# Performance work log

Hardware: AMD Instinct MI355X
Metric: run time of the kernel (lower is better)

The kernel has to match this reference:

```python
import jax, jax.numpy as jnp
import numpy as np
import math

NTOKEN = 32000; D = 512; H = 8; DFF = 2048; L = 4; B = 4; S = 1024; EPS = 1e-5


def _ln(x, g, b):
    m = x.mean(-1, keepdims=True)
    v = ((x - m) ** 2).mean(-1, keepdims=True)
    return (x - m) * jax.lax.rsqrt(v + EPS) * g + b


def setup_inputs() -> dict:
    key = jax.random.key(0)
    ks = jax.random.split(key, 20)
    s = 0.02
    rn = lambda k, shape: jax.random.normal(k, shape, jnp.float32) * s
    return {
        "src": jax.random.randint(ks[0], (B, S), 0, NTOKEN, jnp.int32),
        "emb": rn(ks[1], (NTOKEN, D)),
        "conv_w": rn(ks[2], (D, 1, 3)), "conv_b": rn(ks[3], (D,)),
        "bn_g": jnp.ones((D,)), "bn_b": jnp.zeros((D,)),
        "bn_m": jnp.zeros((D,)), "bn_v": jnp.ones((D,)),
        "w_ih": rn(ks[4], (4 * D, D)), "w_hh": rn(ks[5], (4 * D, D)),
        "b_ih": rn(ks[6], (4 * D,)), "b_hh": rn(ks[7], (4 * D,)),
        "in_w": rn(ks[8], (L, 3 * D, D)), "in_b": rn(ks[9], (L, 3 * D)),
        "out_w": rn(ks[10], (L, D, D)), "out_b": rn(ks[11], (L, D)),
        "ln1_g": jnp.ones((L, D)), "ln1_b": jnp.zeros((L, D)),
        "w1": rn(ks[12], (L, DFF, D)), "b1": rn(ks[13], (L, DFF)),
        "w2": rn(ks[14], (L, D, DFF)), "b2": rn(ks[15], (L, D)),
        "ln2_g": jnp.ones((L, D)), "ln2_b": jnp.zeros((L, D)),
        "fin_g": jnp.ones((D,)), "fin_b": jnp.zeros((D,)),
    }


def _forward(src, emb, conv_w, conv_b, bn_g, bn_b, bn_m, bn_v,
             w_ih, w_hh, b_ih, b_hh, in_w, in_b, out_w, out_b,
             ln1_g, ln1_b, w1, b1, w2, b2, ln2_g, ln2_b, fin_g, fin_b):
    d = emb.shape[1]
    x = emb[src] * math.sqrt(d)  # [B,S,D]
    # sinusoidal positional encoding (dropout is identity at eval)
    pos = jnp.arange(S, dtype=jnp.float32)[:, None]
    div = jnp.exp(jnp.arange(0, d, 2, dtype=jnp.float32) * (-math.log(10000.0) / d))
    pe = jnp.zeros((S, d), jnp.float32)
    pe = pe.at[:, 0::2].set(jnp.sin(pos * div)).at[:, 1::2].set(jnp.cos(pos * div))
    x = x + pe[None]
    # depthwise conv k=3 + BatchNorm1d (eval stats) + ReLU
    xc = jnp.transpose(x, (0, 2, 1))  # [B,D,S]
    xc = jax.lax.conv_general_dilated(xc, conv_w, (1,), [(1, 1)],
                                      feature_group_count=d,
                                      dimension_numbers=('NCH', 'OIH', 'NCH'))
    xc = xc + conv_b[None, :, None]
    xc = (xc - bn_m[None, :, None]) * jax.lax.rsqrt(bn_v + EPS)[None, :, None] \
         * bn_g[None, :, None] + bn_b[None, :, None]
    x = jnp.transpose(jax.nn.relu(xc), (0, 2, 1))
    # single-layer LSTM (torch gate order i,f,g,o)
    def step(carry, xt):
        h, c = carry
        gates = xt @ w_ih.T + b_ih + h @ w_hh.T + b_hh
        i, f, g, o = jnp.split(gates, 4, axis=-1)
        c = jax.nn.sigmoid(f) * c + jax.nn.sigmoid(i) * jnp.tanh(g)
        h = jax.nn.sigmoid(o) * jnp.tanh(c)
        return (h, c), h
    h0 = jnp.zeros((x.shape[0], d), x.dtype)
    _, hs = jax.lax.scan(step, (h0, h0), jnp.transpose(x, (1, 0, 2)))
    x = x + jnp.transpose(hs, (1, 0, 2))
    # post-norm encoder layers, attn weights averaged over heads
    hd = d // H
    scale = 1.0 / math.sqrt(hd)
    attns = []
    out = x
    for l in range(L):
        qkv = out @ in_w[l].T + in_b[l]
        q, k, v = jnp.split(qkv, 3, axis=-1)
        q = q.reshape(B, S, H, hd).transpose(0, 2, 1, 3) * scale
        k = k.reshape(B, S, H, hd).transpose(0, 2, 1, 3)
        v = v.reshape(B, S, H, hd).transpose(0, 2, 1, 3)
        a = jax.nn.softmax(jnp.einsum('bhqd,bhkd->bhqk', q, k), axis=-1)
        attns.append(a.mean(axis=1))  # averaged over heads, as need_weights=True default
        ctx = jnp.einsum('bhqk,bhkd->bhqd', a, v).transpose(0, 2, 1, 3).reshape(B, S, d)
        out = _ln(out + ctx @ out_w[l].T + out_b[l], ln1_g[l], ln1_b[l])
        ff = jax.nn.gelu(out @ w1[l].T + b1[l], approximate=False) @ w2[l].T + b2[l]
        out = _ln(out + ff, ln2_g[l], ln2_b[l])
    return _ln(out, fin_g, fin_b), jnp.stack(attns)


def reference(src, emb, conv_w, conv_b, bn_g, bn_b, bn_m, bn_v,
              w_ih, w_hh, b_ih, b_hh, in_w, in_b, out_w, out_b,
              ln1_g, ln1_b, w1, b1, w2, b2, ln2_g, ln2_b, fin_g, fin_b):
    return _forward(src, emb, conv_w, conv_b, bn_g, bn_b, bn_m, bn_v,
                    w_ih, w_hh, b_ih, b_hh, in_w, in_b, out_w, out_b,
                    ln1_g, ln1_b, w1, b1, w2, b2, ln2_g, ln2_b, fin_g, fin_b)
```

## Files before the change

kernel.cpp:

```cpp
#include <hip/hip_runtime.h>
#include <math.h>

#define DD 512
#define SS 1024
#define BB 4
#define HH 8
#define DFF 2048
#define LL 4
#define NT 4096
#define EPSF 1e-5f

#define O_X0    ((size_t)0)
#define O_X1    ((size_t)2097152)
#define O_HSEQ  ((size_t)4194304)
#define O_CTX   ((size_t)6293504)
#define O_QKV   ((size_t)8390656)
#define O_BIG   ((size_t)14682112)
#define O_BSUM  ((size_t)31459328)

typedef unsigned int  u32;
typedef unsigned short u16;
typedef __attribute__((ext_vector_type(8))) _Float16 f16x8;
typedef __attribute__((ext_vector_type(4))) _Float16 f16x4;
typedef __attribute__((ext_vector_type(4))) float    f32x4;

__device__ __forceinline__ float fsig(float x){
  return __builtin_amdgcn_rcpf(1.0f + __expf(-x));
}
__device__ __forceinline__ float ftanh(float x){
  return 1.0f - 2.0f*__builtin_amdgcn_rcpf(1.0f + __expf(2.0f*x));
}
union f16u { u16 u; _Float16 f; };
__device__ __forceinline__ float b2f(u16 b){ f16u t; t.u = b; return (float)t.f; }
__device__ __forceinline__ u16 f2b(_Float16 h){ f16u t; t.f = h; return t.u; }
__device__ __forceinline__ u32 pack2(float v){
  _Float16 hi = (_Float16)v;
  _Float16 lo = (_Float16)(v - (float)hi);
  return (u32)f2b(hi) | ((u32)f2b(lo) << 16);
}

__global__ void k_embed(const int* __restrict__ src, const float* __restrict__ emb,
                        float* __restrict__ x){
  int idx = blockIdx.x*256 + threadIdx.x;
  if (idx >= NT*DD) return;
  int d = idx & (DD-1);
  int n = idx >> 9;
  int s = n & (SS-1);
  int tok = src[n];
  int i2 = d & ~1;
  float div = expf(-(float)i2 * (9.210340371976184f/512.0f));
  float ang = (float)s * div;
  float pe = (d & 1) ? cosf(ang) : sinf(ang);
  x[idx] = emb[(size_t)tok*DD + d]*22.62741699796952f + pe;
}

__global__ void k_conv(const float* __restrict__ x, const float* __restrict__ cw,
                       const float* __restrict__ cb, const float* __restrict__ bg,
                       const float* __restrict__ bb, const float* __restrict__ bm,
                       const float* __restrict__ bv, float* __restrict__ y,
                       u32* __restrict__ yp){
  int idx = blockIdx.x*256 + threadIdx.x;
  if (idx >= NT*DD) return;
  int d = idx & (DD-1);
  int n = idx >> 9;
  int s = n & (SS-1);
  float acc = cb[d];
  if (s > 0)     acc += x[idx - DD]*cw[d*3+0];
  acc += x[idx]*cw[d*3+1];
  if (s < SS-1)  acc += x[idx + DD]*cw[d*3+2];
  float v = (acc - bm[d])*rsqrtf(bv[d]+EPSF)*bg[d] + bb[d];
  v = fmaxf(v, 0.0f);
  y[idx] = v;
  yp[idx] = pack2(v);
}

__global__ void k_bsum(const float* a, const float* b, float* o, int n){
  int i = blockIdx.x*256 + threadIdx.x;
  if (i < n) o[i] = a[i] + b[i];
}

__global__ void k_wsplit(const float* __restrict__ W, u32* __restrict__ Wp, int total){
  int i = blockIdx.x*1024 + threadIdx.x*4;
  if (i >= total) return;
  float4 v = *reinterpret_cast<const float4*>(W + i);
  uint4 o;
  o.x = pack2(v.x); o.y = pack2(v.y); o.z = pack2(v.z); o.w = pack2(v.w);
  *reinterpret_cast<uint4*>(Wp + i) = o;
}

__global__ void k_wsplit_qkv(const float* __restrict__ inw, const float* __restrict__ inb,
                             u32* __restrict__ Wq, float* __restrict__ qbias){
  size_t i = (size_t)blockIdx.x*1024 + threadIdx.x*4;
  float s = (i < 262144) ? 0.125f : 1.0f;
  float4 v = *reinterpret_cast<const float4*>(inw + i);
  uint4 o;
  o.x = pack2(v.x*s); o.y = pack2(v.y*s); o.z = pack2(v.z*s); o.w = pack2(v.w*s);
  *reinterpret_cast<uint4*>(Wq + i) = o;
  if (blockIdx.x == 0){
    for (int j = threadIdx.x; j < 1536; j += 256){
      float bv = inb[j];
      qbias[j] = (j < 512) ? bv*0.125f : bv;
    }
  }
}

__global__ void k_wsplit_post(const float* __restrict__ outw, const float* __restrict__ w1,
                              const float* __restrict__ w2,
                              u32* __restrict__ Wo, u32* __restrict__ W1p,
                              u32* __restrict__ W2p){
  size_t i = (size_t)blockIdx.x*1024 + threadIdx.x*4;
  const float* src; u32* dst; size_t off;
  if (i < 262144){ src = outw; dst = Wo; off = i; }
  else if (i < 1310720){ src = w1; dst = W1p; off = i - 262144; }
  else { src = w2; dst = W2p; off = i - 1310720; }
  float4 v = *reinterpret_cast<const float4*>(src + off);
  uint4 o;
  o.x = pack2(v.x); o.y = pack2(v.y); o.z = pack2(v.z); o.w = pack2(v.w);
  *reinterpret_cast<uint4*>(dst + off) = o;
}

__device__ __forceinline__ void unpk4(uint4 w, uint2& hi, uint2& lo){
  hi.x = (w.x & 0xffffu) | (w.y << 16);
  hi.y = (w.z & 0xffffu) | (w.w << 16);
  lo.x = (w.x >> 16) | (w.y & 0xffff0000u);
  lo.y = (w.z >> 16) | (w.w & 0xffff0000u);
}
__device__ __forceinline__ uint2 unpk4hi(uint4 w){
  uint2 hi;
  hi.x = (w.x & 0xffffu) | (w.y << 16);
  hi.y = (w.z & 0xffffu) | (w.w << 16);
  return hi;
}

#define BKP 40
template<int ACT, int OSPLIT>
__global__ __launch_bounds__(256) void k_gemm_mfma(const u32* __restrict__ Ain,
                                                   const u32* __restrict__ Wp,
                                                   const float* __restrict__ bias,
                                                   void* __restrict__ Cout,
                                                   int M, int N, int K){
  __shared__ _Float16 Ah[128][BKP];
  __shared__ _Float16 Wh[128][BKP];
  __shared__ _Float16 Wl[128][BKP];
  const int tid = threadIdx.x;
  const int nbx = N >> 7;
  const int bx = blockIdx.x % nbx;
  const int by = blockIdx.x / nbx;
  const int m0 = by << 7, n0 = bx << 7;
  const int lane = tid & 63;
  const int wid  = tid >> 6;
  const int wr = wid >> 1, wc = wid & 1;
  const int fm = lane & 15, fg = lane >> 4;
  const int r0 = tid >> 3;
  const int k4 = (tid & 7) << 2;
  const u32* Wbase = Wp + (size_t)(n0 + r0)*K + k4;
  const u32* Abase = Ain + (size_t)(m0 + r0)*K + k4;

  f32x4 acc[4][4];
  #pragma unroll
  for (int i=0;i<4;i++)
    #pragma unroll
    for (int j=0;j<4;j++) acc[i][j] = (f32x4){0.0f,0.0f,0.0f,0.0f};

  uint4 rw[4], ra4[4];
  #pragma unroll
  for (int e=0;e<4;e++){
    rw[e]  = *reinterpret_cast<const uint4*>(Wbase + (size_t)(e*32)*K);
    ra4[e] = *reinterpret_cast<const uint4*>(Abase + (size_t)(e*32)*K);
  }

  for (int k0 = 0; k0 < K; k0 += 32){
    #pragma unroll
    for (int e = 0; e < 4; ++e){
      int rr = r0 + e*32;
      uint2 hi, lo;
      unpk4(rw[e], hi, lo);
      *reinterpret_cast<uint2*>(&Wh[rr][k4]) = hi;
      *reinterpret_cast<uint2*>(&Wl[rr][k4]) = lo;
      *reinterpret_cast<uint2*>(&Ah[rr][k4]) = unpk4hi(ra4[e]);
    }
    __syncthreads();
    if (k0 + 32 < K){
      #pragma unroll
      for (int e=0;e<4;e++){
        rw[e]  = *reinterpret_cast<const uint4*>(Wbase + (size_t)(e*32)*K + k0 + 32);
        ra4[e] = *reinterpret_cast<const uint4*>(Abase + (size_t)(e*32)*K + k0 + 32);
      }
    }
    f16x8 a_h[4], w_h[4], w_l[4];
    #pragma unroll
    for (int i=0;i<4;i++){
      int row = wr*64 + i*16 + fm;
      a_h[i] = *reinterpret_cast<const f16x8*>(&Ah[row][fg*8]);
    }
    #pragma unroll
    for (int j=0;j<4;j++){
      int row = wc*64 + j*16 + fm;
      w_h[j] = *reinterpret_cast<const f16x8*>(&Wh[row][fg*8]);
      w_l[j] = *reinterpret_cast<const f16x8*>(&Wl[row][fg*8]);
    }
    #pragma unroll
    for (int i=0;i<4;i++)
      #pragma unroll
      for (int j=0;j<4;j++){
        acc[i][j] = __builtin_amdgcn_mfma_f32_16x16x32_f16(a_h[i], w_h[j], acc[i][j], 0, 0, 0);
        acc[i][j] = __builtin_amdgcn_mfma_f32_16x16x32_f16(a_h[i], w_l[j], acc[i][j], 0, 0, 0);
      }
    __syncthreads();
  }
  #pragma unroll
  for (int i=0;i<4;i++){
    #pragma unroll
    for (int r=0;r<4;r++){
      int row = m0 + wr*64 + i*16 + fg*4 + r;
      #pragma unroll
      for (int j=0;j<4;j++){
        int col = n0 + wc*64 + j*16 + fm;
        float v = acc[i][j][r] + bias[col];
        if (ACT == 1) v = 0.5f*v*(1.0f + erff(v*0.70710678118654752f));
        if constexpr (OSPLIT) ((u32*)Cout)[(size_t)row*N + col] = pack2(v);
        else                  ((float*)Cout)[(size_t)row*N + col] = v;
      }
    }
  }
}

template<int ACT, int OSPLIT>
__global__ __launch_bounds__(256) void k_gemm64_mfma(const u32* __restrict__ Ain,
                                                     const u32* __restrict__ Wp,
                                                     const float* __restrict__ bias,
                                                     void* __restrict__ Cout,
                                                     int M, int N, int K){
  __shared__ _Float16 Ah[128][BKP];
  __shared__ _Float16 Wh[64][BKP];
  __shared__ _Float16 Wl[64][BKP];
  const int tid = threadIdx.x;
  const int nbx = N >> 6;
  const int bx = blockIdx.x % nbx;
  const int by = blockIdx.x / nbx;
  const int m0 = by << 7, n0 = bx << 6;
  const int lane = tid & 63;
  const int wid  = tid >> 6;
  const int wr = wid >> 1, wc = wid & 1;
  const int fm = lane & 15, fg = lane >> 4;
  const int r0 = tid >> 3;
  const int k4 = (tid & 7) << 2;
  const u32* Wbase = Wp + (size_t)(n0 + r0)*K + k4;
  const u32* Abase = Ain + (size_t)(m0 + r0)*K + k4;

  f32x4 acc[4][2];
  #pragma unroll
  for (int i=0;i<4;i++){ acc[i][0] = (f32x4){0,0,0,0}; acc[i][1] = (f32x4){0,0,0,0}; }

  uint4 rw[2], ra4[4];
  #pragma unroll
  for (int e=0;e<2;e++)
    rw[e]  = *reinterpret_cast<const uint4*>(Wbase + (size_t)(e*32)*K);
  #pragma unroll
  for (int e=0;e<4;e++)
    ra4[e] = *reinterpret_cast<const uint4*>(Abase + (size_t)(e*32)*K);

  for (int k0 = 0; k0 < K; k0 += 32){
    #pragma unroll
    for (int e = 0; e < 2; ++e){
      int rr = r0 + e*32;
      uint2 hi, lo;
      unpk4(rw[e], hi, lo);
      *reinterpret_cast<uint2*>(&Wh[rr][k4]) = hi;
      *reinterpret_cast<uint2*>(&Wl[rr][k4]) = lo;
    }
    #pragma unroll
    for (int e = 0; e < 4; ++e){
      int rr = r0 + e*32;
      *reinterpret_cast<uint2*>(&Ah[rr][k4]) = unpk4hi(ra4[e]);
    }
    __syncthreads();
    if (k0 + 32 < K){
      #pragma unroll
      for (int e=0;e<2;e++)
        rw[e]  = *reinterpret_cast<const uint4*>(Wbase + (size_t)(e*32)*K + k0 + 32);
      #pragma unroll
      for (int e=0;e<4;e++)
        ra4[e] = *reinterpret_cast<const uint4*>(Abase + (size_t)(e*32)*K + k0 + 32);
    }
    f16x8 a_h[4], w_h[2], w_l[2];
    #pragma unroll
    for (int i=0;i<4;i++){
      int row = wr*64 + i*16 + fm;
      a_h[i] = *reinterpret_cast<const f16x8*>(&Ah[row][fg*8]);
    }
    #pragma unroll
    for (int j=0;j<2;j++){
      int row = wc*32 + j*16 + fm;
      w_h[j] = *reinterpret_cast<const f16x8*>(&Wh[row][fg*8]);
      w_l[j] = *reinterpret_cast<const f16x8*>(&Wl[row][fg*8]);
    }
    #pragma unroll
    for (int i=0;i<4;i++)
      #pragma unroll
      for (int j=0;j<2;j++){
        acc[i][j] = __builtin_amdgcn_mfma_f32_16x16x32_f16(a_h[i], w_h[j], acc[i][j], 0, 0, 0);
        acc[i][j] = __builtin_amdgcn_mfma_f32_16x16x32_f16(a_h[i], w_l[j], acc[i][j], 0, 0, 0);
      }
    __syncthreads();
  }
  #pragma unroll
  for (int i=0;i<4;i++){
    #pragma unroll
    for (int r=0;r<4;r++){
      int row = m0 + wr*64 + i*16 + fg*4 + r;
      #pragma unroll
      for (int j=0;j<2;j++){
        int col = n0 + wc*32 + j*16 + fm;
        float v = acc[i][j][r] + bias[col];
        if (ACT == 1) v = 0.5f*v*(1.0f + erff(v*0.70710678118654752f));
        if constexpr (OSPLIT) ((u32*)Cout)[(size_t)row*N + col] = pack2(v);
        else                  ((float*)Cout)[(size_t)row*N + col] = v;
      }
    }
  }
}

#define SPAD 72
__global__ __launch_bounds__(256) void k_scores_mfma(const u32* __restrict__ qkv,
                                                     u16* __restrict__ sc){
  __shared__ _Float16 Qh[128][SPAD];
  __shared__ _Float16 Kh[128][SPAD], Kl[128][SPAD];
  const int tid = threadIdx.x;
  const int kt = blockIdx.x & 7;
  const int qt = (blockIdx.x >> 3) & 7;
  const int h  = (blockIdx.x >> 6) & 7;
  const int b  = (blockIdx.x >> 9) & 3;
  const int q0 = qt*128, k0 = kt*128;
  #pragma unroll
  for (int e=0;e<8;e++){
    int lin = e*256 + tid;
    int rr = lin >> 4;
    int c4 = (lin & 15) << 2;
    uint4 qv = *reinterpret_cast<const uint4*>(qkv + (size_t)(b*SS + q0+rr)*1536 + h*64 + c4);
    uint4 kv = *reinterpret_cast<const uint4*>(qkv + (size_t)(b*SS + k0+rr)*1536 + DD + h*64 + c4);
    uint2 hi, lo;
    *reinterpret_cast<uint2*>(&Qh[rr][c4]) = unpk4hi(qv);
    unpk4(kv, hi, lo);
    *reinterpret_cast<uint2*>(&Kh[rr][c4]) = hi;
    *reinterpret_cast<uint2*>(&Kl[rr][c4]) = lo;
  }
  __syncthreads();
  const int lane = tid & 63, wid = tid >> 6;
  const int wr = wid >> 1, wc = wid & 1;
  const int fm = lane & 15, fg = lane >> 4;
  f32x4 acc[4][4];
  #pragma unroll
  for (int i=0;i<4;i++)
    #pragma unroll
    for (int j=0;j<4;j++) acc[i][j] = (f32x4){0.0f,0.0f,0.0f,0.0f};
  #pragma unroll
  for (int ks=0; ks<2; ks++){
    f16x8 ah[4], bh[4], bl[4];
    #pragma unroll
    for (int i=0;i<4;i++){
      int row = wr*64 + i*16 + fm;
      ah[i] = *reinterpret_cast<const f16x8*>(&Qh[row][ks*32 + fg*8]);
    }
    #pragma unroll
    for (int j=0;j<4;j++){
      int row = wc*64 + j*16 + fm;
      bh[j] = *reinterpret_cast<const f16x8*>(&Kh[row][ks*32 + fg*8]);
      bl[j] = *reinterpret_cast<const f16x8*>(&Kl[row][ks*32 + fg*8]);
    }
    #pragma unroll
    for (int i=0;i<4;i++)
      #pragma unroll
      for (int j=0;j<4;j++){
        acc[i][j] = __builtin_amdgcn_mfma_f32_16x16x32_f16(ah[i], bh[j], acc[i][j], 0, 0, 0);
        acc[i][j] = __builtin_amdgcn_mfma_f32_16x16x32_f16(ah[i], bl[j], acc[i][j], 0, 0, 0);
      }
  }
  u16* out = sc + (size_t)(b*HH + h)*SS*SS;
  #pragma unroll
  for (int i=0;i<4;i++){
    #pragma unroll
    for (int r=0;r<4;r++){
      int row = q0 + wr*64 + i*16 + fg*4 + r;
      #pragma unroll
      for (int j=0;j<4;j++){
        int col = k0 + wc*64 + j*16 + fm;
        out[(size_t)row*SS + col] = f2b((_Float16)acc[i][j][r]);
      }
    }
  }
}

__global__ __launch_bounds__(256) void k_pv_mfma(const u16* __restrict__ sc,
                                                 const u32* __restrict__ qkv,
                                                 u32* __restrict__ ctx){
  __shared__ _Float16 Ph[64][SPAD];
  __shared__ _Float16 Vh[64][SPAD],  Vl[64][SPAD];
  const int tid = threadIdx.x;
  const int qt = blockIdx.x & 15;
  const int h  = (blockIdx.x >> 4) & 7;
  const int b  = (blockIdx.x >> 7) & 3;
  const int q0 = qt*64;
  const u16* Pb = sc + (size_t)(b*HH + h)*SS*SS;
  const int lane = tid & 63, wid = tid >> 6;
  const int wr = wid >> 1, wc = wid & 1;
  const int fm = lane & 15, fg = lane >> 4;
  const int pr0 = tid >> 4;
  const int pc4 = (tid & 15) << 2;
  const int vd  = tid & 63;
  const int vk0 = tid >> 6;
  const u16* Pbase = Pb + (size_t)(q0 + pr0)*SS + pc4;
  const u32* Vbase = qkv + (size_t)(b*SS + vk0)*1536 + 1024 + h*64 + vd;
  f32x4 acc[2][2];
  #pragma unroll
  for (int i=0;i<2;i++){ acc[i][0] = (f32x4){0,0,0,0}; acc[i][1] = (f32x4){0,0,0,0}; }

  uint2 rp[4];
  u32   rv[16];
  #pragma unroll
  for (int e=0;e<4;e++)  rp[e] = *reinterpret_cast<const uint2*>(Pbase + (size_t)(e*16)*SS);
  #pragma unroll
  for (int e=0;e<16;e++) rv[e] = Vbase[(size_t)(e*4)*1536];

  for (int kk0=0; kk0<SS; kk0+=64){
    #pragma unroll
    for (int e=0;e<4;e++){
      int rr = pr0 + e*16;
      *reinterpret_cast<uint2*>(&Ph[rr][pc4]) = rp[e];
    }
    #pragma unroll
    for (int e=0;e<16;e++){
      int k = vk0 + e*4;
      u32 w = rv[e];
      f16u thi, tlo; thi.u = (u16)w; tlo.u = (u16)(w >> 16);
      Vh[vd][k] = thi.f;
      Vl[vd][k] = tlo.f;
    }
    __syncthreads();
    if (kk0 + 64 < SS){
      #pragma unroll
      for (int e=0;e<4;e++)
        rp[e] = *reinterpret_cast<const uint2*>(Pbase + (size_t)(e*16)*SS + kk0 + 64);
      #pragma unroll
      for (int e=0;e<16;e++)
        rv[e] = Vbase[(size_t)(kk0 + 64 + e*4)*1536];
    }
    #pragma unroll
    for (int ks=0; ks<2; ks++){
      f16x8 ah[2], bh[2], bl[2];
      #pragma unroll
      for (int i=0;i<2;i++){
        int row = wr*32 + i*16 + fm;
        ah[i] = *reinterpret_cast<const f16x8*>(&Ph[row][ks*32 + fg*8]);
      }
      #pragma unroll
      for (int j=0;j<2;j++){
        int row = wc*32 + j*16 + fm;
        bh[j] = *reinterpret_cast<const f16x8*>(&Vh[row][ks*32 + fg*8]);
        bl[j] = *reinterpret_cast<const f16x8*>(&Vl[row][ks*32 + fg*8]);
      }
      #pragma unroll
      for (int i=0;i<2;i++)
        #pragma unroll
        for (int j=0;j<2;j++){
          acc[i][j] = __builtin_amdgcn_mfma_f32_16x16x32_f16(ah[i], bh[j], acc[i][j], 0, 0, 0);
          acc[i][j] = __builtin_amdgcn_mfma_f32_16x16x32_f16(ah[i], bl[j], acc[i][j], 0, 0, 0);
        }
    }
    __syncthreads();
  }
  #pragma unroll
  for (int i=0;i<2;i++){
    #pragma unroll
    for (int r=0;r<4;r++){
      int row = q0 + wr*32 + i*16 + fg*4 + r;
      #pragma unroll
      for (int j=0;j<2;j++){
        int col = wc*32 + j*16 + fm;
        ctx[(size_t)(b*SS + row)*DD + h*64 + col] = pack2(acc[i][j][r]);
      }
    }
  }
}

__global__ __launch_bounds__(256) void k_lstm(const float* __restrict__ gates_in,
                                              const float* __restrict__ w_hh,
                                              unsigned long long* __restrict__ hpack){
  __shared__ float hsh[2][8][68];
  const int b = blockIdx.x >> 6;
  const int chunk = blockIdx.x & 63;
  const int d0 = chunk*8;
  const int tid = threadIdx.x;
  const int wave = tid >> 6;
  const int lane = tid & 63;
  const int diw = lane >> 5;
  const int g   = (lane >> 3) & 3;
  const int ks  = lane & 7;
  const int dim = wave*2 + diw;
  const int src0 = diw*32;
  float w[64];
  {
    const float* wrow = w_hh + (size_t)(g*DD + d0 + dim)*DD;
// ... 41 lines not shown
    float acc = (a0+a1)+(a2+a3);
    acc += __shfl_down(acc, 4, 8);
    acc += __shfl_down(acc, 2, 8);
    acc += __shfl_down(acc, 1, 8);
    float v = acc + gv;
    float gval = (g == 2) ? ftanh(v) : fsig(v);
    float gi = __shfl(gval, src0 + 0);
    float gf = __shfl(gval, src0 + 8);
    float gg = __shfl(gval, src0 + 16);
    float go = __shfl(gval, src0 + 24);
    c = gf*c + gi*gg;
    float h = go*ftanh(c);
    if (lane == src0){
      union { float f; unsigned int u; } hu; hu.f = h;
      unsigned long long pk = ((unsigned long long)(unsigned int)(t+1) << 32)
                            | (unsigned long long)hu.u;
      __hip_atomic_store(&hpack[(size_t)((t+1)*BB + b)*DD + d0 + dim], pk,
                         __ATOMIC_RELAXED, __HIP_MEMORY_SCOPE_AGENT);
    }
  }
}

__global__ void k_resid(float* __restrict__ x, const unsigned long long* __restrict__ hpack,
                        u32* __restrict__ xp){
  int idx = blockIdx.x*256 + threadIdx.x;
  if (idx >= NT*DD) return;
  int d = idx & (DD-1);
  int n = idx >> 9;
  int s = n & (SS-1);
  int b = n >> 10;
  union { unsigned int u; float f; } hu;
  hu.u = (unsigned int)hpack[(size_t)((s+1)*BB + b)*DD + d];
  float v = x[idx] + hu.f;
  x[idx] = v;
  xp[idx] = pack2(v);
}

__global__ __launch_bounds__(256) void k_softmax(u16* __restrict__ sc,
                                                 float* __restrict__ attn_out,
                                                 int l){
  __shared__ float avgw[4][SS];
  const int tid = threadIdx.x;
  const int q  = blockIdx.x & (SS-1);
  const int b  = blockIdx.x >> 10;
  const int wave = tid >> 6, lane = tid & 63;
  #pragma unroll
  for (int j=0;j<16;j++) avgw[wave][j*64 + lane] = 0.0f;
  #pragma unroll
  for (int hi=0; hi<2; hi++){
    int h = wave + hi*4;
    u16* row = sc + (size_t)(b*HH + h)*SS*SS + (size_t)q*SS;
    float v[16];
    float m = -1e30f;
    #pragma unroll
    for (int j=0;j<16;j++){ v[j] = b2f(row[j*64 + lane]); m = fmaxf(m, v[j]); }
    #pragma unroll
    for (int o=32;o>0;o>>=1) m = fmaxf(m, __shfl_xor(m, o));
    float s = 0.0f;
    #pragma unroll
    for (int j=0;j<16;j++){ v[j] = __expf(v[j] - m); s += v[j]; }
    #pragma unroll
    for (int o=32;o>0;o>>=1) s += __shfl_xor(s, o);
    float inv = __builtin_amdgcn_rcpf(s);
    #pragma unroll
    for (int j=0;j<16;j++){
      float p = v[j]*inv;
      row[j*64 + lane] = f2b((_Float16)p);
      avgw[wave][j*64 + lane] += p;
    }
  }
  __syncthreads();
  float* ao = attn_out + (size_t)((l*BB + b)*SS + q)*SS;
  for (int j=tid;j<SS;j+=256)
    ao[j] = (avgw[0][j]+avgw[1][j]+avgw[2][j]+avgw[3][j])*0.125f;
}

__global__ __launch_bounds__(64) void k_ln(const float* __restrict__ x,
                                           const float* __restrict__ y,
                                           const float* __restrict__ g,
                                           const float* __restrict__ bta,
                                           float* __restrict__ out,
                                           u32* __restrict__ outp){
  const int n = blockIdx.x;
  const int tid = threadIdx.x;
  float v[8];
  float s = 0.0f, sq = 0.0f;
  #pragma unroll
  for (int j=0;j<8;j++){
    int d = j*64 + tid;
    float a = x[(size_t)n*DD + d];
    if (y) a += y[(size_t)n*DD + d];
    v[j] = a; s += a; sq += a*a;
  }
  #pragma unroll
  for (int o=32;o>0;o>>=1){ s += __shfl_xor(s, o); sq += __shfl_xor(sq, o); }
  float mean = s*(1.0f/DD);
  float var = sq*(1.0f/DD) - mean*mean;
  float rstd = rsqrtf(var + EPSF);
  #pragma unroll
  for (int j=0;j<8;j++){
    int d = j*64 + tid;
    float r = (v[j]-mean)*rstd*g[d] + bta[d];
    out[(size_t)n*DD + d] = r;
    if (outp) outp[(size_t)n*DD + d] = pack2(r);
  }
}

extern "C" void kernel_launch(void* const* d_in, const int* in_sizes, int n_in,
                              void* d_out, int out_size, void* d_ws, size_t ws_size,
                              hipStream_t stream){
  const int*   src    = (const int*)  d_in[0];
  const float* emb    = (const float*)d_in[1];
  const float* conv_w = (const float*)d_in[2];
  const float* conv_b = (const float*)d_in[3];
  const float* bn_g   = (const float*)d_in[4];
  const float* bn_b   = (const float*)d_in[5];
  const float* bn_m   = (const float*)d_in[6];
  const float* bn_v   = (const float*)d_in[7];
  const float* w_ih   = (const float*)d_in[8];
  const float* w_hh   = (const float*)d_in[9];
  const float* b_ih   = (const float*)d_in[10];
  const float* b_hh   = (const float*)d_in[11];
  const float* in_w   = (const float*)d_in[12];
  const float* in_b   = (const float*)d_in[13];
  const float* out_w  = (const float*)d_in[14];
  const float* out_b  = (const float*)d_in[15];
  const float* ln1_g  = (const float*)d_in[16];
  const float* ln1_b  = (const float*)d_in[17];
  const float* w1     = (const float*)d_in[18];
  const float* b1     = (const float*)d_in[19];
  const float* w2     = (const float*)d_in[20];
  const float* b2     = (const float*)d_in[21];
  const float* ln2_g  = (const float*)d_in[22];
  const float* ln2_b  = (const float*)d_in[23];
  const float* fin_g  = (const float*)d_in[24];
  const float* fin_b  = (const float*)d_in[25];

  float* ws    = (float*)d_ws;
  float* x0    = ws + O_X0;
  float* x1    = ws + O_X1;
  float* ctx   = ws + O_CTX;
  float* qkv   = ws + O_QKV;
  float* big   = ws + O_BIG;
  float* bsum  = ws + O_BSUM;
  unsigned long long* hpack = (unsigned long long*)(big + 8388608);

  u32*   aconv = (u32*)(ws + O_HSEQ);
  float* qbias = ws + O_HSEQ + 2097152;
  u32*   qkvp  = (u32*)qkv;
  u32*   ctxp  = (u32*)ctx;
  u16*   sc16  = (u16*)big;
  u32*   wsg   = (u32*)(big + 13000000);
  u32*   Wq    = (u32*)(big + 8388608);
  u32*   Wo    = (u32*)(big + 8388608);
  u32*   W1p   = (u32*)(big + 8650752);
  u32*   W2p   = (u32*)(big + 9699328);

  float* outx  = (float*)d_out;
  float* attn  = outx + (size_t)NT*DD;

  hipMemsetAsync(hpack, 0, (size_t)(SS+1)*BB*DD*sizeof(unsigned long long), stream);

  const int eb = (NT*DD)/256;
  k_embed<<<eb, 256, 0, stream>>>(src, emb, x0);
  k_conv <<<eb, 256, 0, stream>>>(x0, conv_w, conv_b, bn_g, bn_b, bn_m, bn_v, x1, aconv);
  k_bsum <<<8, 256, 0, stream>>>(b_ih, b_hh, bsum, 4*DD);

  k_wsplit<<<1024, 256, 0, stream>>>(w_ih, wsg, 2048*512);
  k_gemm_mfma<0,0><<<(NT/128)*((4*DD)/128), 256, 0, stream>>>(
      aconv, wsg, bsum, big, NT, 4*DD, DD);
  k_lstm<<<256, 256, 0, stream>>>(big, w_hh, hpack);
  k_resid<<<eb, 256, 0, stream>>>(x1, hpack, aconv);

  float* cur = x1;
  float* tmp = x0;
  for (int l=0; l<LL; ++l){
    k_wsplit_qkv<<<768, 256, 0, stream>>>(in_w + (size_t)l*1536*DD,
                                          in_b + (size_t)l*1536, Wq, qbias);
    k_gemm_mfma<0,1><<<(NT/128)*(1536/128), 256, 0, stream>>>(
        aconv, Wq, qbias, qkvp, NT, 1536, DD);
    k_scores_mfma<<<2048, 256, 0, stream>>>(qkvp, sc16);
    k_softmax    <<<4096, 256, 0, stream>>>(sc16, attn, l);
    k_pv_mfma    <<<512,  256, 0, stream>>>(sc16, qkvp, ctxp);
    k_wsplit_post<<<2304, 256, 0, stream>>>(out_w + (size_t)l*DD*DD,
                                            w1 + (size_t)l*DFF*DD,
                                            w2 + (size_t)l*DD*DFF, Wo, W1p, W2p);
    k_gemm64_mfma<0,0><<<(NT/128)*(DD/64), 256, 0, stream>>>(
        ctxp, Wo, out_b + (size_t)l*DD, tmp, NT, DD, DD);
    k_ln<<<NT, 64, 0, stream>>>(cur, tmp, ln1_g + l*DD, ln1_b + l*DD, cur, aconv);
    k_gemm_mfma<1,1><<<(NT/128)*(DFF/128), 256, 0, stream>>>(
        aconv, W1p, b1 + (size_t)l*DFF, (u32*)big, NT, DFF, DD);
    k_gemm64_mfma<0,0><<<(NT/128)*(DD/64), 256, 0, stream>>>(
        (u32*)big, W2p, b2 + (size_t)l*DD, tmp, NT, DD, DFF);
    k_ln<<<NT, 64, 0, stream>>>(cur, tmp, ln2_g + l*DD, ln2_b + l*DD, cur, aconv);
  }
  k_ln<<<NT, 64, 0, stream>>>(cur, nullptr, fin_g, fin_b, outx, nullptr);
}
```

Measured before the change: 2.481 ms.

## Drop split-fp16 low parts for transformer GEMMs and attention, use plain fp16

Activations, QKV, context, FFN hidden and transformer weights are stored as single fp16 values instead of packed hi/lo fp16 pairs. The low-part MFMA passes in the attention and FFN GEMMs, scores and PV kernels are removed, which halves MFMA work and shared/global traffic for those stages. Only the LSTM input projection keeps a split-precision weight. The QKV GEMM also moves to the 64-wide tile kernel. Numerical accuracy falls to plain fp16 inputs with fp32 accumulation, which could exceed tolerance.

```diff
diff --git a/kernel.cpp b/kernel.cpp
--- a/kernel.cpp
+++ b/kernel.cpp
@@ -21,7 +21,6 @@
 typedef unsigned int  u32;
 typedef unsigned short u16;
 typedef __attribute__((ext_vector_type(8))) _Float16 f16x8;
-typedef __attribute__((ext_vector_type(4))) _Float16 f16x4;
 typedef __attribute__((ext_vector_type(4))) float    f32x4;
 
 __device__ __forceinline__ float fsig(float x){
@@ -37,6 +36,12 @@
   _Float16 hi = (_Float16)v;
   _Float16 lo = (_Float16)(v - (float)hi);
   return (u32)f2b(hi) | ((u32)f2b(lo) << 16);
+}
+__device__ __forceinline__ uint2 pk4h(float4 v, float s){
+  uint2 o;
+  o.x = (u32)f2b((_Float16)(v.x*s)) | ((u32)f2b((_Float16)(v.y*s)) << 16);
+  o.y = (u32)f2b((_Float16)(v.z*s)) | ((u32)f2b((_Float16)(v.w*s)) << 16);
+  return o;
 }
 
 __global__ void k_embed(const int* __restrict__ src, const float* __restrict__ emb,
@@ -58,7 +63,7 @@
                        const float* __restrict__ cb, const float* __restrict__ bg,
                        const float* __restrict__ bb, const float* __restrict__ bm,
                        const float* __restrict__ bv, float* __restrict__ y,
-                       u32* __restrict__ yp){
+                       u16* __restrict__ yp){
   int idx = blockIdx.x*256 + threadIdx.x;
   if (idx >= NT*DD) return;
   int d = idx & (DD-1);
@@ -71,7 +76,7 @@
   float v = (acc - bm[d])*rsqrtf(bv[d]+EPSF)*bg[d] + bb[d];
   v = fmaxf(v, 0.0f);
   y[idx] = v;
-  yp[idx] = pack2(v);
+  yp[idx] = f2b((_Float16)v);
 }
 
 __global__ void k_bsum(const float* a, const float* b, float* o, int n){
@@ -89,13 +94,11 @@
 }
 
 __global__ void k_wsplit_qkv(const float* __restrict__ inw, const float* __restrict__ inb,
-                             u32* __restrict__ Wq, float* __restrict__ qbias){
+                             u16* __restrict__ Wq, float* __restrict__ qbias){
   size_t i = (size_t)blockIdx.x*1024 + threadIdx.x*4;
   float s = (i < 262144) ? 0.125f : 1.0f;
   float4 v = *reinterpret_cast<const float4*>(inw + i);
-  uint4 o;
-  o.x = pack2(v.x*s); o.y = pack2(v.y*s); o.z = pack2(v.z*s); o.w = pack2(v.w*s);
-  *reinterpret_cast<uint4*>(Wq + i) = o;
+  *reinterpret_cast<uint2*>(Wq + i) = pk4h(v, s);
   if (blockIdx.x == 0){
     for (int j = threadIdx.x; j < 1536; j += 256){
       float bv = inb[j];
@@ -106,17 +109,15 @@
 
 __global__ void k_wsplit_post(const float* __restrict__ outw, const float* __restrict__ w1,
                               const float* __restrict__ w2,
-                              u32* __restrict__ Wo, u32* __restrict__ W1p,
-                              u32* __restrict__ W2p){
+                              u16* __restrict__ Wo, u16* __restrict__ W1p,
+                              u16* __restrict__ W2p){
   size_t i = (size_t)blockIdx.x*1024 + threadIdx.x*4;
-  const float* src; u32* dst; size_t off;
+  const float* src; u16* dst; size_t off;
   if (i < 262144){ src = outw; dst = Wo; off = i; }
   else if (i < 1310720){ src = w1; dst = W1p; off = i - 262144; }
   else { src = w2; dst = W2p; off = i - 1310720; }
   float4 v = *reinterpret_cast<const float4*>(src + off);
-  uint4 o;
-  o.x = pack2(v.x); o.y = pack2(v.y); o.z = pack2(v.z); o.w = pack2(v.w);
-  *reinterpret_cast<uint4*>(dst + off) = o;
+  *reinterpret_cast<uint2*>(dst + off) = pk4h(v, 1.0f);
 }
 
 __device__ __forceinline__ void unpk4(uint4 w, uint2& hi, uint2& lo){
@@ -125,20 +126,14 @@
   lo.x = (w.x >> 16) | (w.y & 0xffff0000u);
   lo.y = (w.z >> 16) | (w.w & 0xffff0000u);
 }
-__device__ __forceinline__ uint2 unpk4hi(uint4 w){
-  uint2 hi;
-  hi.x = (w.x & 0xffffu) | (w.y << 16);
-  hi.y = (w.z & 0xffffu) | (w.w << 16);
-  return hi;
-}
 
 #define BKP 40
-template<int ACT, int OSPLIT>
-__global__ __launch_bounds__(256) void k_gemm_mfma(const u32* __restrict__ Ain,
-                                                   const u32* __restrict__ Wp,
-                                                   const float* __restrict__ bias,
-                                                   void* __restrict__ Cout,
-                                                   int M, int N, int K){
+
+__global__ __launch_bounds__(256) void k_gemm2p(const u16* __restrict__ A,
+                                                const u32* __restrict__ Wp,
+                                                const float* __restrict__ bias,
+                                                float* __restrict__ C,
+                                                int M, int N, int K){
   __shared__ _Float16 Ah[128][BKP];
   __shared__ _Float16 Wh[128][BKP];
   __shared__ _Float16 Wl[128][BKP];
@@ -151,10 +146,12 @@
   const int wid  = tid >> 6;
   const int wr = wid >> 1, wc = wid & 1;
   const int fm = lane & 15, fg = lane >> 4;
-  const int r0 = tid >> 3;
-  const int k4 = (tid & 7) << 2;
-  const u32* Wbase = Wp + (size_t)(n0 + r0)*K + k4;
-  const u32* Abase = Ain + (size_t)(m0 + r0)*K + k4;
+  const int r0a = tid >> 2;
+  const int k8  = (tid & 3) << 3;
+  const int r0w = tid >> 3;
+  const int k4  = (tid & 7) << 2;
+  const u16* Abase = A + (size_t)(m0 + r0a)*K + k8;
+  const u32* Wbase = Wp + (size_t)(n0 + r0w)*K + k4;
 
   f32x4 acc[4][4];
   #pragma unroll
@@ -162,42 +159,40 @@
     #pragma unroll
     for (int j=0;j<4;j++) acc[i][j] = (f32x4){0.0f,0.0f,0.0f,0.0f};
 
-  uint4 rw[4], ra4[4];
-  #pragma unroll
-  for (int e=0;e<4;e++){
-    rw[e]  = *reinterpret_cast<const uint4*>(Wbase + (size_t)(e*32)*K);
-    ra4[e] = *reinterpret_cast<const uint4*>(Abase + (size_t)(e*32)*K);
-  }
+  uint4 ra[2], rw[4];
+  #pragma unroll
+  for (int e=0;e<2;e++) ra[e] = *reinterpret_cast<const uint4*>(Abase + (size_t)(e*64)*K);
+  #pragma unroll
+  for (int e=0;e<4;e++) rw[e] = *reinterpret_cast<const uint4*>(Wbase + (size_t)(e*32)*K);
 
   for (int k0 = 0; k0 < K; k0 += 32){
     #pragma unroll
-    for (int e = 0; e < 4; ++e){
-      int rr = r0 + e*32;
+    for (int e=0;e<2;e++)
+      *reinterpret_cast<uint4*>(&Ah[r0a + e*64][k8]) = ra[e];
+    #pragma unroll
+    for (int e=0;e<4;e++){
       uint2 hi, lo;
       unpk4(rw[e], hi, lo);
-      *reinterpret_cast<uint2*>(&Wh[rr][k4]) = hi;
-      *reinterpret_cast<uint2*>(&Wl[rr][k4]) = lo;
-      *reinterpret_cast<uint2*>(&Ah[rr][k4]) = unpk4hi(ra4[e]);
+      *reinterpret_cast<uint2*>(&Wh[r0w + e*32][k4]) = hi;
+      *reinterpret_cast<uint2*>(&Wl[r0w + e*32][k4]) = lo;
     }
     __syncthreads();
     if (k0 + 32 < K){
       #pragma unroll
-      for (int e=0;e<4;e++){
-        rw[e]  = *reinterpret_cast<const uint4*>(Wbase + (size_t)(e*32)*K + k0 + 32);
-        ra4[e] = *reinterpret_cast<const uint4*>(Abase + (size_t)(e*32)*K + k0 + 32);
-      }
+      for (int e=0;e<2;e++)
+        ra[e] = *reinterpret_cast<const uint4*>(Abase + (size_t)(e*64)*K + k0 + 32);
+      #pragma unroll
+      for (int e=0;e<4;e++)
+        rw[e] = *reinterpret_cast<const uint4*>(Wbase + (size_t)(e*32)*K + k0 + 32);
     }
     f16x8 a_h[4], w_h[4], w_l[4];
     #pragma unroll
-    for (int i=0;i<4;i++){
-      int row = wr*64 + i*16 + fm;
-      a_h[i] = *reinterpret_cast<const f16x8*>(&Ah[row][fg*8]);
-    }
+    for (int i=0;i<4;i++)
+      a_h[i] = *reinterpret_cast<const f16x8*>(&Ah[wr*64 + i*16 + fm][fg*8]);
     #pragma unroll
     for (int j=0;j<4;j++){
-      int row = wc*64 + j*16 + fm;
-      w_h[j] = *reinterpret_cast<const f16x8*>(&Wh[row][fg*8]);
-      w_l[j] = *reinterpret_cast<const f16x8*>(&Wl[row][fg*8]);
+      w_h[j] = *reinterpret_cast<const f16x8*>(&Wh[wc*64 + j*16 + fm][fg*8]);
+      w_l[j] = *reinterpret_cast<const f16x8*>(&Wl[wc*64 + j*16 + fm][fg*8]);
     }
     #pragma unroll
     for (int i=0;i<4;i++)
@@ -216,24 +211,100 @@
       #pragma unroll
       for (int j=0;j<4;j++){
         int col = n0 + wc*64 + j*16 + fm;
+        C[(size_t)row*N + col] = acc[i][j][r] + bias[col];
+      }
+    }
+  }
+}
+
+template<int ACT, int OHALF>
+__global__ __launch_bounds__(256) void k_gemmh(const u16* __restrict__ A,
+                                               const u16* __restrict__ W,
+                                               const float* __restrict__ bias,
+                                               void* __restrict__ Cout,
+                                               int M, int N, int K){
+  __shared__ _Float16 Ah[128][BKP];
+  __shared__ _Float16 Wh[128][BKP];
+  const int tid = threadIdx.x;
+  const int nbx = N >> 7;
+  const int bx = blockIdx.x % nbx;
+  const int by = blockIdx.x / nbx;
+  const int m0 = by << 7, n0 = bx << 7;
+  const int lane = tid & 63;
+  const int wid  = tid >> 6;
+  const int wr = wid >> 1, wc = wid & 1;
+  const int fm = lane & 15, fg = lane >> 4;
+  const int r0 = tid >> 2;
+  const int k8 = (tid & 3) << 3;
+  const u16* Abase = A + (size_t)(m0 + r0)*K + k8;
+  const u16* Wbase = W + (size_t)(n0 + r0)*K + k8;
+
+  f32x4 acc[4][4];
+  #pragma unroll
+  for (int i=0;i<4;i++)
+    #pragma unroll
+    for (int j=0;j<4;j++) acc[i][j] = (f32x4){0.0f,0.0f,0.0f,0.0f};
+
+  uint4 ra[2], rw[2];
+  #pragma unroll
+  for (int e=0;e<2;e++){
+    ra[e] = *reinterpret_cast<const uint4*>(Abase + (size_t)(e*64)*K);
+    rw[e] = *reinterpret_cast<const uint4*>(Wbase + (size_t)(e*64)*K);
+  }
+
+  for (int k0 = 0; k0 < K; k0 += 32){
+    #pragma unroll
+    for (int e=0;e<2;e++){
+      *reinterpret_cast<uint4*>(&Ah[r0 + e*64][k8]) = ra[e];
+      *reinterpret_cast<uint4*>(&Wh[r0 + e*64][k8]) = rw[e];
+    }
+    __syncthreads();
+    if (k0 + 32 < K){
+      #pragma unroll
+      for (int e=0;e<2;e++){
+        ra[e] = *reinterpret_cast<const uint4*>(Abase + (size_t)(e*64)*K + k0 + 32);
+        rw[e] = *reinterpret_cast<const uint4*>(Wbase + (size_t)(e*64)*K + k0 + 32);
+      }
+    }
+    f16x8 a_h[4], w_h[4];
+    #pragma unroll
+    for (int i=0;i<4;i++)
+      a_h[i] = *reinterpret_cast<const f16x8*>(&Ah[wr*64 + i*16 + fm][fg*8]);
+    #pragma unroll
+    for (int j=0;j<4;j++)
+      w_h[j] = *reinterpret_cast<const f16x8*>(&Wh[wc*64 + j*16 + fm][fg*8]);
+    #pragma unroll
+    for (int i=0;i<4;i++)
+      #pragma unroll
+      for (int j=0;j<4;j++)
+        acc[i][j] = __builtin_amdgcn_mfma_f32_16x16x32_f16(a_h[i], w_h[j], acc[i][j], 0, 0, 0);
+    __syncthreads();
+  }
+  #pragma unroll
+  for (int i=0;i<4;i++){
+    #pragma unroll
+    for (int r=0;r<4;r++){
+      int row = m0 + wr*64 + i*16 + fg*4 + r;
+      #pragma unroll
+      for (int j=0;j<4;j++){
+        int col = n0 + wc*64 + j*16 + fm;
         float v = acc[i][j][r] + bias[col];
         if (ACT == 1) v = 0.5f*v*(1.0f + erff(v*0.70710678118654752f));
-        if constexpr (OSPLIT) ((u32*)Cout)[(size_t)row*N + col] = pack2(v);
-        else                  ((float*)Cout)[(size_t)row*N + col] = v;
+        if constexpr (OHALF) ((u16*)Cout)[(size_t)row*N + col] = f2b((_Float16)v);
+        else                 ((float*)Cout)[(size_t)row*N + col] = v;
       }
     }
   }
 }
 
-template<int ACT, int OSPLIT>
-__global__ __launch_bounds__(256) void k_gemm64_mfma(const u32* __restrict__ Ain,
-                                                     const u32* __restrict__ Wp,
-                                                     const float* __restrict__ bias,
-                                                     void* __restrict__ Cout,
-                                                     int M, int N, int K){
+template<int ACT, int OHALF>
+__global__ __launch_bounds__(256) void k_gemm64h(const u16* __restrict__ A,
+                                                 const u16* __restrict__ W,
+                                                 const float* __restrict__ bias,
+                                                 void* __restrict__ Cout,
+                                                 int M, int N, int K){
   __shared__ _Float16 Ah[128][BKP];
   __shared__ _Float16 Wh[64][BKP];
-  __shared__ _Float16 Wl[64][BKP];
   const int tid = threadIdx.x;
   const int nbx = N >> 6;
   const int bx = blockIdx.x % nbx;
@@ -243,65 +314,45 @@
   const int wid  = tid >> 6;
   const int wr = wid >> 1, wc = wid & 1;
   const int fm = lane & 15, fg = lane >> 4;
-  const int r0 = tid >> 3;
-  const int k4 = (tid & 7) << 2;
-  const u32* Wbase = Wp + (size_t)(n0 + r0)*K + k4;
-  const u32* Abase = Ain + (size_t)(m0 + r0)*K + k4;
+  const int r0 = tid >> 2;
+  const int k8 = (tid & 3) << 3;
+  const u16* Abase = A + (size_t)(m0 + r0)*K + k8;
+  const u16* Wbase = W + (size_t)(n0 + r0)*K + k8;
 
   f32x4 acc[4][2];
   #pragma unroll
   for (int i=0;i<4;i++){ acc[i][0] = (f32x4){0,0,0,0}; acc[i][1] = (f32x4){0,0,0,0}; }
 
-  uint4 rw[2], ra4[4];
+  uint4 ra[2], rw0;
   #pragma unroll
   for (int e=0;e<2;e++)
-    rw[e]  = *reinterpret_cast<const uint4*>(Wbase + (size_t)(e*32)*K);
-  #pragma unroll
-  for (int e=0;e<4;e++)
-    ra4[e] = *reinterpret_cast<const uint4*>(Abase + (size_t)(e*32)*K);
+    ra[e] = *reinterpret_cast<const uint4*>(Abase + (size_t)(e*64)*K);
+  rw0 = *reinterpret_cast<const uint4*>(Wbase);
 
   for (int k0 = 0; k0 < K; k0 += 32){
     #pragma unroll
-    for (int e = 0; e < 2; ++e){
-      int rr = r0 + e*32;
-      uint2 hi, lo;
-      unpk4(rw[e], hi, lo);
-      *reinterpret_cast<uint2*>(&Wh[rr][k4]) = hi;
-      *reinterpret_cast<uint2*>(&Wl[rr][k4]) = lo;
-    }
-    #pragma unroll
-    for (int e = 0; e < 4; ++e){
-      int rr = r0 + e*32;
-      *reinterpret_cast<uint2*>(&Ah[rr][k4]) = unpk4hi(ra4[e]);
-    }
+    for (int e=0;e<2;e++)
+      *reinterpret_cast<uint4*>(&Ah[r0 + e*64][k8]) = ra[e];
+    *reinterpret_cast<uint4*>(&Wh[r0][k8]) = rw0;
     __syncthreads();
     if (k0 + 32 < K){
       #pragma unroll
       for (int e=0;e<2;e++)
-        rw[e]  = *reinterpret_cast<const uint4*>(Wbase + (size_t)(e*32)*K + k0 + 32);
-      #pragma unroll
-      for (int e=0;e<4;e++)
-        ra4[e] = *reinterpret_cast<const uint4*>(Abase + (size_t)(e*32)*K + k0 + 32);
-    }
-    f16x8 a_h[4], w_h[2], w_l[2];
-    #pragma unroll
-    for (int i=0;i<4;i++){
-      int row = wr*64 + i*16 + fm;
-      a_h[i] = *reinterpret_cast<const f16x8*>(&Ah[row][fg*8]);
-    }
-    #pragma unroll
-    for (int j=0;j<2;j++){
-      int row = wc*32 + j*16 + fm;
-      w_h[j] = *reinterpret_cast<const f16x8*>(&Wh[row][fg*8]);
-      w_l[j] = *reinterpret_cast<const f16x8*>(&Wl[row][fg*8]);
-    }
+        ra[e] = *reinterpret_cast<const uint4*>(Abase + (size_t)(e*64)*K + k0 + 32);
+      rw0 = *reinterpret_cast<const uint4*>(Wbase + k0 + 32);
+    }
+    f16x8 a_h[4], w_h[2];
     #pragma unroll
     for (int i=0;i<4;i++)
-      #pragma unroll
-      for (int j=0;j<2;j++){
+      a_h[i] = *reinterpret_cast<const f16x8*>(&Ah[wr*64 + i*16 + fm][fg*8]);
+    #pragma unroll
+    for (int j=0;j<2;j++)
+      w_h[j] = *reinterpret_cast<const f16x8*>(&Wh[wc*32 + j*16 + fm][fg*8]);
+    #pragma unroll
+    for (int i=0;i<4;i++)
+      #pragma unroll
+      for (int j=0;j<2;j++)
         acc[i][j] = __builtin_amdgcn_mfma_f32_16x16x32_f16(a_h[i], w_h[j], acc[i][j], 0, 0, 0);
-        acc[i][j] = __builtin_amdgcn_mfma_f32_16x16x32_f16(a_h[i], w_l[j], acc[i][j], 0, 0, 0);
-      }
     __syncthreads();
   }
   #pragma unroll
@@ -314,18 +365,18 @@
         int col = n0 + wc*32 + j*16 + fm;
         float v = acc[i][j][r] + bias[col];
         if (ACT == 1) v = 0.5f*v*(1.0f + erff(v*0.70710678118654752f));
-        if constexpr (OSPLIT) ((u32*)Cout)[(size_t)row*N + col] = pack2(v);
-        else                  ((float*)Cout)[(size_t)row*N + col] = v;
+        if constexpr (OHALF) ((u16*)Cout)[(size_t)row*N + col] = f2b((_Float16)v);
+        else                 ((float*)Cout)[(size_t)row*N + col] = v;
       }
     }
   }
 }
 
 #define SPAD 72
-__global__ __launch_bounds__(256) void k_scores_mfma(const u32* __restrict__ qkv,
+__global__ __launch_bounds__(256) void k_scores_mfma(const u16* __restrict__ qkv,
                                                      u16* __restrict__ sc){
   __shared__ _Float16 Qh[128][SPAD];
-  __shared__ _Float16 Kh[128][SPAD], Kl[128][SPAD];
+  __shared__ _Float16 Kh[128][SPAD];
   const int tid = threadIdx.x;
   const int kt = blockIdx.x & 7;
   const int qt = (blockIdx.x >> 3) & 7;
@@ -333,17 +384,14 @@
   const int b  = (blockIdx.x >> 9) & 3;
   const int q0 = qt*128, k0 = kt*128;
   #pragma unroll
-  for (int e=0;e<8;e++){
+  for (int e=0;e<4;e++){
     int lin = e*256 + tid;
-    int rr = lin >> 4;
-    int c4 = (lin & 15) << 2;
-    uint4 qv = *reinterpret_cast<const uint4*>(qkv + (size_t)(b*SS + q0+rr)*1536 + h*64 + c4);
-    uint4 kv = *reinterpret_cast<const uint4*>(qkv + (size_t)(b*SS + k0+rr)*1536 + DD + h*64 + c4);
-    uint2 hi, lo;
-    *reinterpret_cast<uint2*>(&Qh[rr][c4]) = unpk4hi(qv);
-    unpk4(kv, hi, lo);
-    *reinterpret_cast<uint2*>(&Kh[rr][c4]) = hi;
-    *reinterpret_cast<uint2*>(&Kl[rr][c4]) = lo;
+    int rr = lin >> 3;
+    int c8 = (lin & 7) << 3;
+    *reinterpret_cast<uint4*>(&Qh[rr][c8]) =
+      *reinterpret_cast<const uint4*>(qkv + (size_t)(b*SS + q0+rr)*1536 + h*64 + c8);
+    *reinterpret_cast<uint4*>(&Kh[rr][c8]) =
+      *reinterpret_cast<const uint4*>(qkv + (size_t)(b*SS + k0+rr)*1536 + DD + h*64 + c8);
   }
   __syncthreads();
   const int lane = tid & 63, wid = tid >> 6;
@@ -356,25 +404,18 @@
     for (int j=0;j<4;j++) acc[i][j] = (f32x4){0.0f,0.0f,0.0f,0.0f};
   #pragma unroll
   for (int ks=0; ks<2; ks++){
-    f16x8 ah[4], bh[4], bl[4];
-    #pragma unroll
-    for (int i=0;i<4;i++){
-      int row = wr*64 + i*16 + fm;
-      ah[i] = *reinterpret_cast<const f16x8*>(&Qh[row][ks*32 + fg*8]);
-    }
-    #pragma unroll
-    for (int j=0;j<4;j++){
-      int row = wc*64 + j*16 + fm;
-      bh[j] = *reinterpret_cast<const f16x8*>(&Kh[row][ks*32 + fg*8]);
-      bl[j] = *reinterpret_cast<const f16x8*>(&Kl[row][ks*32 + fg*8]);
-    }
+    f16x8 ah[4], bh[4];
     #pragma unroll
     for (int i=0;i<4;i++)
-      #pragma unroll
-      for (int j=0;j<4;j++){
+      ah[i] = *reinterpret_cast<const f16x8*>(&Qh[wr*64 + i*16 + fm][ks*32 + fg*8]);
+    #pragma unroll
+    for (int j=0;j<4;j++)
+      bh[j] = *reinterpret_cast<const f16x8*>(&Kh[wc*64 + j*16 + fm][ks*32 + fg*8]);
+    #pragma unroll
+    for (int i=0;i<4;i++)
+      #pragma unroll
+      for (int j=0;j<4;j++)
         acc[i][j] = __builtin_amdgcn_mfma_f32_16x16x32_f16(ah[i], bh[j], acc[i][j], 0, 0, 0);
-        acc[i][j] = __builtin_amdgcn_mfma_f32_16x16x32_f16(ah[i], bl[j], acc[i][j], 0, 0, 0);
-      }
   }
   u16* out = sc + (size_t)(b*HH + h)*SS*SS;
   #pragma unroll
@@ -392,10 +433,10 @@
 }
 
 __global__ __launch_bounds__(256) void k_pv_mfma(const u16* __restrict__ sc,
-                                                 const u32* __restrict__ qkv,
-                                                 u32* __restrict__ ctx){
+                                                 const u16* __restrict__ qkv,
+                                                 u16* __restrict__ ctx){
   __shared__ _Float16 Ph[64][SPAD];
-  __shared__ _Float16 Vh[64][SPAD],  Vl[64][SPAD];
+  __shared__ _Float16 Vh[64][SPAD];
   const int tid = threadIdx.x;
   const int qt = blockIdx.x & 15;
   const int h  = (blockIdx.x >> 4) & 7;
@@ -405,67 +446,55 @@
   const int lane = tid & 63, wid = tid >> 6;
   const int wr = wid >> 1, wc = wid & 1;
   const int fm = lane & 15, fg = lane >> 4;
-  const int pr0 = tid >> 4;
-  const int pc4 = (tid & 15) << 2;
+  const int pr0 = tid >> 3;
+  const int pc8 = (tid & 7) << 3;
   const int vd  = tid & 63;
   const int vk0 = tid >> 6;
-  const u16* Pbase = Pb + (size_t)(q0 + pr0)*SS + pc4;
-  const u32* Vbase = qkv + (size_t)(b*SS + vk0)*1536 + 1024 + h*64 + vd;
+  const u16* Pbase = Pb + (size_t)(q0 + pr0)*SS + pc8;
+  const u16* Vbase = qkv + (size_t)(b*SS + vk0)*1536 + 1024 + h*64 + vd;
   f32x4 acc[2][2];
   #pragma unroll
   for (int i=0;i<2;i++){ acc[i][0] = (f32x4){0,0,0,0}; acc[i][1] = (f32x4){0,0,0,0}; }
 
-  uint2 rp[4];
-  u32   rv[16];
-  #pragma unroll
-  for (int e=0;e<4;e++)  rp[e] = *reinterpret_cast<const uint2*>(Pbase + (size_t)(e*16)*SS);
+  uint4 rp[2];
+  u16   rv[16];
+  #pragma unroll
+  for (int e=0;e<2;e++) rp[e] = *reinterpret_cast<const uint4*>(Pbase + (size_t)(e*32)*SS);
   #pragma unroll
   for (int e=0;e<16;e++) rv[e] = Vbase[(size_t)(e*4)*1536];
 
   for (int kk0=0; kk0<SS; kk0+=64){
     #pragma unroll
-    for (int e=0;e<4;e++){
-      int rr = pr0 + e*16;
-      *reinterpret_cast<uint2*>(&Ph[rr][pc4]) = rp[e];
-    }
+    for (int e=0;e<2;e++)
+      *reinterpret_cast<uint4*>(&Ph[pr0 + e*32][pc8]) = rp[e];
     #pragma unroll
     for (int e=0;e<16;e++){
-      int k = vk0 + e*4;
-      u32 w = rv[e];
-      f16u thi, tlo; thi.u = (u16)w; tlo.u = (u16)(w >> 16);
-      Vh[vd][k] = thi.f;
-      Vl[vd][k] = tlo.f;
+      f16u t; t.u = rv[e];
+      Vh[vd][vk0 + e*4] = t.f;
     }
     __syncthreads();
     if (kk0 + 64 < SS){
       #pragma unroll
-      for (int e=0;e<4;e++)
-        rp[e] = *reinterpret_cast<const uint2*>(Pbase + (size_t)(e*16)*SS + kk0 + 64);
+      for (int e=0;e<2;e++)
+        rp[e] = *reinterpret_cast<const uint4*>(Pbase + (size_t)(e*32)*SS + kk0 + 64);
       #pragma unroll
       for (int e=0;e<16;e++)
         rv[e] = Vbase[(size_t)(kk0 + 64 + e*4)*1536];
     }
     #pragma unroll
     for (int ks=0; ks<2; ks++){
-      f16x8 ah[2], bh[2], bl[2];
-      #pragma unroll
-      for (int i=0;i<2;i++){
-        int row = wr*32 + i*16 + fm;
-        ah[i] = *reinterpret_cast<const f16x8*>(&Ph[row][ks*32 + fg*8]);
-      }
-      #pragma unroll
-      for (int j=0;j<2;j++){
-        int row = wc*32 + j*16 + fm;
-        bh[j] = *reinterpret_cast<const f16x8*>(&Vh[row][ks*32 + fg*8]);
-        bl[j] = *reinterpret_cast<const f16x8*>(&Vl[row][ks*32 + fg*8]);
-      }
+      f16x8 ah[2], bh[2];
+      #pragma unroll
+      for (int i=0;i<2;i++)
+        ah[i] = *reinterpret_cast<const f16x8*>(&Ph[wr*32 + i*16 + fm][ks*32 + fg*8]);
+      #pragma unroll
+      for (int j=0;j<2;j++)
+        bh[j] = *reinterpret_cast<const f16x8*>(&Vh[wc*32 + j*16 + fm][ks*32 + fg*8]);
       #pragma unroll
       for (int i=0;i<2;i++)
         #pragma unroll
-        for (int j=0;j<2;j++){
+        for (int j=0;j<2;j++)
           acc[i][j] = __builtin_amdgcn_mfma_f32_16x16x32_f16(ah[i], bh[j], acc[i][j], 0, 0, 0);
-          acc[i][j] = __builtin_amdgcn_mfma_f32_16x16x32_f16(ah[i], bl[j], acc[i][j], 0, 0, 0);
-        }
     }
     __syncthreads();
   }
@@ -477,7 +506,7 @@
       #pragma unroll
       for (int j=0;j<2;j++){
         int col = wc*32 + j*16 + fm;
-        ctx[(size_t)(b*SS + row)*DD + h*64 + col] = pack2(acc[i][j][r]);
+        ctx[(size_t)(b*SS + row)*DD + h*64 + col] = f2b((_Float16)acc[i][j][r]);
       }
     }
   }
@@ -565,7 +594,7 @@
 }
 
 __global__ void k_resid(float* __restrict__ x, const unsigned long long* __restrict__ hpack,
-                        u32* __restrict__ xp){
+                        u16* __restrict__ xp){
   int idx = blockIdx.x*256 + threadIdx.x;
   if (idx >= NT*DD) return;
   int d = idx & (DD-1);
@@ -576,7 +605,7 @@
   hu.u = (unsigned int)hpack[(size_t)((s+1)*BB + b)*DD + d];
   float v = x[idx] + hu.f;
   x[idx] = v;
-  xp[idx] = pack2(v);
+  xp[idx] = f2b((_Float16)v);
 }
 
 __global__ __launch_bounds__(256) void k_softmax(u16* __restrict__ sc,
@@ -623,7 +652,7 @@
                                            const float* __restrict__ g,
                                            const float* __restrict__ bta,
                                            float* __restrict__ out,
-                                           u32* __restrict__ outp){
+                                           u16* __restrict__ outp){
   const int n = blockIdx.x;
   const int tid = threadIdx.x;
   float v[8];
@@ -645,7 +674,7 @@
     int d = j*64 + tid;
     float r = (v[j]-mean)*rstd*g[d] + bta[d];
     out[(size_t)n*DD + d] = r;
-    if (outp) outp[(size_t)n*DD + d] = pack2(r);
+    if (outp) outp[(size_t)n*DD + d] = f2b((_Float16)r);
   }
 }
 
@@ -682,22 +711,21 @@
   float* ws    = (float*)d_ws;
   float* x0    = ws + O_X0;
   float* x1    = ws + O_X1;
-  float* ctx   = ws + O_CTX;
-  float* qkv   = ws + O_QKV;
   float* big   = ws + O_BIG;
   float* bsum  = ws + O_BSUM;
   unsigned long long* hpack = (unsigned long long*)(big + 8388608);
 
-  u32*   aconv = (u32*)(ws + O_HSEQ);
+  u16*   aconv = (u16*)(ws + O_HSEQ);
   float* qbias = ws + O_HSEQ + 2097152;
-  u32*   qkvp  = (u32*)qkv;
-  u32*   ctxp  = (u32*)ctx;
+  u16*   qkvp  = (u16*)(ws + O_QKV);
+  u16*   ctxp  = (u16*)(ws + O_CTX);
   u16*   sc16  = (u16*)big;
   u32*   wsg   = (u32*)(big + 13000000);
-  u32*   Wq    = (u32*)(big + 8388608);
-  u32*   Wo    = (u32*)(big + 8388608);
-  u32*   W1p   = (u32*)(big + 8650752);
-  u32*   W2p   = (u32*)(big + 9699328);
+  u16*   Wq    = (u16*)(big + 8388608);
+  u16*   Wo    = (u16*)(big + 8388608);
+  u16*   W1p   = (u16*)(big + 8650752);
+  u16*   W2p   = (u16*)(big + 9699328);
+  u16*   ffh   = (u16*)big;
 
   float* outx  = (float*)d_out;
   float* attn  = outx + (size_t)NT*DD;
@@ -710,7 +738,7 @@
   k_bsum <<<8, 256, 0, stream>>>(b_ih, b_hh, bsum, 4*DD);
 
   k_wsplit<<<1024, 256, 0, stream>>>(w_ih, wsg, 2048*512);
-  k_gemm_mfma<0,0><<<(NT/128)*((4*DD)/128), 256, 0, stream>>>(
+  k_gemm2p<<<(NT/128)*((4*DD)/128), 256, 0, stream>>>(
       aconv, wsg, bsum, big, NT, 4*DD, DD);
   k_lstm<<<256, 256, 0, stream>>>(big, w_hh, hpack);
   k_resid<<<eb, 256, 0, stream>>>(x1, hpack, aconv);
@@ -720,7 +748,7 @@
   for (int l=0; l<LL; ++l){
     k_wsplit_qkv<<<768, 256, 0, stream>>>(in_w + (size_t)l*1536*DD,
                                           in_b + (size_t)l*1536, Wq, qbias);
-    k_gemm_mfma<0,1><<<(NT/128)*(1536/128), 256, 0, stream>>>(
+    k_gemm64h<0,1><<<(NT/128)*(1536/64), 256, 0, stream>>>(
         aconv, Wq, qbias, qkvp, NT, 1536, DD);
     k_scores_mfma<<<2048, 256, 0, stream>>>(qkvp, sc16);
     k_softmax    <<<4096, 256, 0, stream>>>(sc16, attn, l);
@@ -728,13 +756,13 @@
     k_wsplit_post<<<2304, 256, 0, stream>>>(out_w + (size_t)l*DD*DD,
                                             w1 + (size_t)l*DFF*DD,
                                             w2 + (size_t)l*DD*DFF, Wo, W1p, W2p);
-    k_gemm64_mfma<0,0><<<(NT/128)*(DD/64), 256, 0, stream>>>(
+    k_gemm64h<0,0><<<(NT/128)*(DD/64), 256, 0, stream>>>(
         ctxp, Wo, out_b + (size_t)l*DD, tmp, NT, DD, DD);
     k_ln<<<NT, 64, 0, stream>>>(cur, tmp, ln1_g + l*DD, ln1_b + l*DD, cur, aconv);
-    k_gemm_mfma<1,1><<<(NT/128)*(DFF/128), 256, 0, stream>>>(
-        aconv, W1p, b1 + (size_t)l*DFF, (u32*)big, NT, DFF, DD);
-    k_gemm64_mfma<0,0><<<(NT/128)*(DD/64), 256, 0, stream>>>(
-        (u32*)big, W2p, b2 + (size_t)l*DD, tmp, NT, DD, DFF);
+    k_gemmh<1,1><<<(NT/128)*(DFF/128), 256, 0, stream>>>(
+        aconv, W1p, b1 + (size_t)l*DFF, ffh, NT, DFF, DD);
+    k_gemm64h<0,0><<<(NT/128)*(DD/64), 256, 0, stream>>>(
+        ffh, W2p, b2 + (size_t)l*DD, tmp, NT, DD, DFF);
     k_ln<<<NT, 64, 0, stream>>>(cur, tmp, ln2_g + l*DD, ln2_b + l*DD, cur, aconv);
   }
   k_ln<<<NT, 64, 0, stream>>>(cur, nullptr, fin_g, fin_b, outx, nullptr);
```

Measured after the change: 2.596 ms. 1.05x slower.
